# Kernel tuning notes

Measured on AMD Instinct MI355X. Metric: run time of the kernel, lower is better.

The kernel has to match this reference:

```python
import jax, jax.numpy as jnp
import numpy as np

NPG = 400          # nodes per graph (CC400 atlas ROIs)
B = 512            # graphs per batch
N = B * NPG        # total nodes
EPG = 6400         # edges per graph (avg degree 16)
E = B * EPG
F_IN = 200         # node feature dim
H = 64             # hidden_channels
C = 2              # num_classes


def _lin(k, fi, fo):
    return jax.random.normal(k, (fi, fo), jnp.float32) / np.sqrt(fi)


def setup_inputs() -> dict:
    key = jax.random.key(0)
    ks = jax.random.split(key, 16)
    # intra-graph edges: local src/dst in [0, NPG) plus per-graph offset
    g = jnp.repeat(jnp.arange(B, dtype=jnp.int32), EPG)
    src = jax.random.randint(ks[0], (E,), 0, NPG, dtype=jnp.int32) + g * NPG
    dst = jax.random.randint(ks[1], (E,), 0, NPG, dtype=jnp.int32) + g * NPG
    edge_index = jnp.stack([src, dst])  # [2, E]
    x = jax.random.normal(ks[2], (N, F_IN), jnp.float32)
    return dict(
        x=x, edge_index=edge_index, npg=NPG,
        # SAGEConv i: out = lin_l(mean_agg) + lin_r(x); lin_l carries the bias
        W1l=_lin(ks[3], F_IN, H), W1r=_lin(ks[4], F_IN, H), b1=jnp.zeros((H,), jnp.float32),
        W2l=_lin(ks[5], H, H), W2r=_lin(ks[6], H, H), b2=jnp.zeros((H,), jnp.float32),
        W3l=_lin(ks[7], H, H), W3r=_lin(ks[8], H, H), b3=jnp.zeros((H,), jnp.float32),
        # SAGPooling score GNN = GraphConv(H, 1): lin_rel(sum_agg) + lin_root(x)
        Wpr=_lin(ks[9], H, 1), bpr=jnp.zeros((1,), jnp.float32), Wpo=_lin(ks[10], H, 1),
        # final classifier
        Wlin=_lin(ks[11], H, C), blin=jnp.zeros((C,), jnp.float32),
    )


def reference(x, edge_index, npg, W1l, W1r, b1, W2l, W2r, b2, W3l, W3r, b3,
              Wpr, bpr, Wpo, Wlin, blin):
    n = x.shape[0]
    src, dst = edge_index[0], edge_index[1]

    deg = jax.ops.segment_sum(jnp.ones((src.shape[0],), x.dtype), dst, num_segments=n)
    inv_deg = 1.0 / jnp.maximum(deg, 1.0)  # [n]

    def sage(h, Wl, Wr, b):
        # mean aggregation over incoming edges, then lin_l(agg)+b + lin_r(h)
        agg = jax.ops.segment_sum(h[src], dst, num_segments=n) * inv_deg[:, None]
        return agg @ Wl + b + h @ Wr

    x1 = jax.nn.relu(sage(x, W1l, W1r, b1))
    x2 = jax.nn.relu(sage(x1, W2l, W2r, b2)) + x1
    x3 = jax.nn.relu(sage(x2, W3l, W3r, b3)) + x2

    # SAGPooling score via GraphConv (add aggregation)
    score = (jax.ops.segment_sum(x3[src], dst, num_segments=n) @ Wpr + bpr
             + x3 @ Wpo)[:, 0]  # [n]

    nb = n // npg            # number of graphs
    k = npg // 2             # ratio = 0.5, uniform graph sizes
    vals, idx = jax.lax.top_k(score.reshape(nb, npg), k)       # [nb, k]
    flat_idx = (jnp.arange(nb, dtype=idx.dtype)[:, None] * npg + idx).reshape(-1)
    xp = x3[flat_idx] * jnp.tanh(vals.reshape(-1))[:, None]    # [nb*k, H]

    pooled = xp.reshape(nb, k, -1).mean(axis=1)                # global_mean_pool
    logits = pooled @ Wlin + blin
    return jax.nn.log_softmax(logits, axis=1)
```

## Files before the change

### kernel.cpp

```cpp
#include <hip/hip_runtime.h>
#include <hip/hip_bf16.h>
#include <math.h>

#define F_IN 200
#define HDIM 64
#define NPG  400
#define EPG  6400
#define KSEL 200

typedef __attribute__((ext_vector_type(4))) float f32x4;
typedef __attribute__((ext_vector_type(8))) short s16x8;

__device__ __forceinline__ void gload_lds16(const void* g, void* l) {
    __builtin_amdgcn_global_load_lds(
        (const __attribute__((address_space(1))) void*)g,
        (__attribute__((address_space(3))) void*)l, 16, 0, 0);
}

__device__ __forceinline__ unsigned int bf16_rne(float x) {
    unsigned int b = __float_as_uint(x);
    return (b + 0x7FFFu + ((b >> 16) & 1u)) >> 16;
}

__device__ __forceinline__ void split8(f32x4 v0, f32x4 v1, s16x8& h, s16x8& l) {
    float x[8] = {v0.x, v0.y, v0.z, v0.w, v1.x, v1.y, v1.z, v1.w};
#pragma unroll
    for (int j = 0; j < 8; j++) {
        unsigned int hb = bf16_rne(x[j]);
        float hf = __uint_as_float(hb << 16);
        float r = x[j] - hf;
        unsigned int lb = bf16_rne(r);
        h[j] = (short)hb;
        l[j] = (short)lb;
    }
}

__global__ void pack_wf(const float* __restrict__ Wl, const float* __restrict__ Wr,
                        short* __restrict__ WF, int K, int KC) {
    int idx = blockIdx.x * blockDim.x + threadIdx.x;
    if (idx >= KC * 4096) return;
    int j    = idx & 7;
    int lane = (idx >> 3) & 63;
    int nf   = (idx >> 9) & 7;
    int kc   = idx >> 12;
    int k = kc * 32 + (lane >> 4) * 8 + j;
    int n = nf * 16 + (lane & 15);
    float v = 0.f;
    if (k < K) v = (n < 64) ? Wl[k * 64 + n] : Wr[k * 64 + (n - 64)];
    unsigned int hb = bf16_rne(v);
    float hf = __uint_as_float(hb << 16);
    unsigned int lb = bf16_rne(v - hf);
    WF[(size_t)((kc * 8 + nf) * 2 + 0) * 512 + lane * 8 + j] = (short)hb;
    WF[(size_t)((kc * 8 + nf) * 2 + 1) * 512 + lane * 8 + j] = (short)lb;
}

__global__ void pack_wf4(const float* __restrict__ Wl, const float* __restrict__ Wr,
                         short* __restrict__ WF) {
    int idx = blockIdx.x * blockDim.x + threadIdx.x;
    if (idx >= 4 * 2048) return;
    int j    = idx & 7;
    int lane = (idx >> 3) & 63;
    int nf   = (idx >> 9) & 3;
    int kc   = idx >> 11;
    int k = kc * 32 + (lane >> 4) * 8 + j;
    int n = nf * 16 + (lane & 15);
    float v = (k < 64) ? Wl[k * 64 + n] : Wr[(k - 64) * 64 + n];
    unsigned int hb = bf16_rne(v);
    float hf = __uint_as_float(hb << 16);
    unsigned int lb = bf16_rne(v - hf);
    WF[(size_t)((kc * 4 + nf) * 2 + 0) * 512 + lane * 8 + j] = (short)hb;
    WF[(size_t)((kc * 4 + nf) * 2 + 1) * 512 + lane * 8 + j] = (short)lb;
}

template <int K, int LDX, int KC, int TAIL>
__global__ __launch_bounds__(256) void gemm_lds(const float* __restrict__ X,
                                                const short* __restrict__ WF,
                                                float* __restrict__ O) {
    __shared__ float Xs[2][128 * 32];
    __shared__ short Ws[2][8 * 2 * 512];
    const int tid  = threadIdx.x;
    const int lane = tid & 63;
    const int wave = tid >> 6;
    const size_t rowbase = (size_t)blockIdx.x * 128;
    const f32x4 zero4 = (f32x4){0.f, 0.f, 0.f, 0.f};

    const int srow_off = wave * 32 + (lane >> 3);
    const int sbyte    = 16 * ((lane & 7) ^ (lane >> 3));

#define DMA_CHUNK(b, kc_) {                                                      \
    _Pragma("unroll")                                                            \
    for (int j = 0; j < 4; j++) {                                                \
        const char* xsrc = (const char*)X +                                      \
            (rowbase + srow_off + j * 8) * (size_t)(LDX * 4) + (kc_) * 128 + sbyte; \
        gload_lds16(xsrc, (char*)&Xs[b][0] + wave * 4096 + j * 1024);            \
        const short* wsrc = WF + (size_t)(kc_) * 8192 + wave * 2048 + j * 512 + lane * 8; \
        gload_lds16(wsrc, (char*)&Ws[b][0] + wave * 4096 + j * 1024);            \
    } }

    f32x4 acc[2][8];
#pragma unroll
    for (int m = 0; m < 2; m++)
#pragma unroll
        for (int nf = 0; nf < 8; nf++) acc[m][nf] = zero4;

    DMA_CHUNK(0, 0);
    __syncthreads();

    for (int kc = 0; kc < KC; kc++) {
        const int b = kc & 1;
        if (kc + 1 < KC) DMA_CHUNK(b ^ 1, kc + 1);

        s16x8 ah[2], al[2];
#pragma unroll
        for (int m = 0; m < 2; m++) {
            const int lr = wave * 32 + m * 16 + (lane & 15);
            const int g0 = (lane >> 4) * 2;
            f32x4 v0 = *(const f32x4*)&Xs[b][lr * 32 + 4 * (g0 ^ (lane & 7))];
            f32x4 v1 = *(const f32x4*)&Xs[b][lr * 32 + 4 * ((g0 + 1) ^ (lane & 7))];
            split8(v0, v1, ah[m], al[m]);
        }
#pragma unroll
        for (int nf = 0; nf < 8; nf++) {
            s16x8 wh = *(const s16x8*)&Ws[b][(nf * 2 + 0) * 512 + lane * 8];
            s16x8 wl = *(const s16x8*)&Ws[b][(nf * 2 + 1) * 512 + lane * 8];
#pragma unroll
            for (int m = 0; m < 2; m++) {
                acc[m][nf] = __builtin_amdgcn_mfma_f32_16x16x32_bf16(ah[m], wh, acc[m][nf], 0, 0, 0);
                acc[m][nf] = __builtin_amdgcn_mfma_f32_16x16x32_bf16(al[m], wh, acc[m][nf], 0, 0, 0);
                acc[m][nf] = __builtin_amdgcn_mfma_f32_16x16x32_bf16(ah[m], wl, acc[m][nf], 0, 0, 0);
            }
        }
        __syncthreads();
    }
#undef DMA_CHUNK

    if constexpr (TAIL > 0) {
        s16x8 ah[2], al[2];
#pragma unroll
        for (int m = 0; m < 2; m++) {
            const size_t row = rowbase + wave * 32 + m * 16 + (lane & 15);
            const int k0 = KC * 32 + (lane >> 4) * 8;
            f32x4 v0 = (k0 + 4 <= K) ? *(const f32x4*)&X[row * (size_t)LDX + k0] : zero4;
            f32x4 v1 = (k0 + 8 <= K) ? *(const f32x4*)&X[row * (size_t)LDX + k0 + 4] : zero4;
            split8(v0, v1, ah[m], al[m]);
        }
#pragma unroll
        for (int nf = 0; nf < 8; nf++) {
            s16x8 wh = *(const s16x8*)&WF[(size_t)((KC * 8 + nf) * 2 + 0) * 512 + lane * 8];
            s16x8 wl = *(const s16x8*)&WF[(size_t)((KC * 8 + nf) * 2 + 1) * 512 + lane * 8];
#pragma unroll
            for (int m = 0; m < 2; m++) {
                acc[m][nf] = __builtin_amdgcn_mfma_f32_16x16x32_bf16(ah[m], wh, acc[m][nf], 0, 0, 0);
                acc[m][nf] = __builtin_amdgcn_mfma_f32_16x16x32_bf16(al[m], wh, acc[m][nf], 0, 0, 0);
                acc[m][nf] = __builtin_amdgcn_mfma_f32_16x16x32_bf16(ah[m], wl, acc[m][nf], 0, 0, 0);
            }
        }
    }

    float* cs0 = &Xs[0][wave * 1024];
    float* cs1 = &Xs[1][wave * 1024];
#pragma unroll
    for (int m = 0; m < 2; m++) {
        const int scol = lane & 15;
        const int srow = (lane >> 4) * 4;
#pragma unroll
        for (int nf = 0; nf < 8; nf++)
#pragma unroll
            for (int r = 0; r < 4; r++) {
                int cr = srow + r;
                float* p = (cr < 8) ? cs0 + cr * 128 : cs1 + (cr - 8) * 128;
                p[nf * 16 + scol] = acc[m][nf][r];
            }
#pragma unroll
        for (int ps = 0; ps < 8; ps++) {
            int row = ps * 2 + (lane >> 5);
            const float* p = (row < 8) ? cs0 + row * 128 : cs1 + (row - 8) * 128;
            f32x4 v = *(const f32x4*)&p[(lane & 31) * 4];
            *(f32x4*)&O[(rowbase + wave * 32 + m * 16 + row) * 128 + (lane & 31) * 4] = v;
        }
    }
}

__global__ __launch_bounds__(1024) void combine_gemm(
    const float* __restrict__ M, const float* __restrict__ H,
    const short* __restrict__ WF, const float* __restrict__ bias,
    const float* __restrict__ resid, float* __restrict__ P)
{
    __shared__ float Xs[2][256 * 32];
    __shared__ short Ws[2][4 * 2 * 512];
    const int tid  = threadIdx.x;
    const int lane = tid & 63;
    const int wave = tid >> 6;
    const size_t rowbase = (size_t)blockIdx.x * 256;

#define DMA_C(b, c_) {                                                           \
    const float* srcbuf_ = ((c_) < 2) ? M : H;                                   \
    _Pragma("unroll")                                                            \
    for (int i = 0; i < 2; i++) {                                                \
        int rr = i * 8 + (lane >> 3);                                            \
        int jj = (lane & 7) ^ (rr & 7);                                          \
        const char* src = (const char*)(srcbuf_ + (rowbase + wave * 16 + rr) * 64) \
                          + ((c_) & 1) * 128 + jj * 16;                          \
        gload_lds16(src, (char*)&Xs[b][0] + wave * 2048 + i * 1024 + lane * 16); \
    }                                                                            \
    if (tid < 512) {                                                             \
        const short* wsrc = WF + (size_t)(c_) * 4096 + tid * 8;                  \
        gload_lds16(wsrc, (char*)&Ws[b][0] + tid * 16);                          \
    } }

    f32x4 acc[4];
#pragma unroll
    for (int nf = 0; nf < 4; nf++) acc[nf] = (f32x4){0.f, 0.f, 0.f, 0.f};

    DMA_C(0, 0);
    __syncthreads();

    for (int c = 0; c < 4; c++) {
        const int b = c & 1;
        if (c + 1 < 4) DMA_C(b ^ 1, c + 1);

        const int r = lane & 15;
        const int j0 = (lane >> 4) * 2;
        const float* abase = &Xs[b][wave * 512 + r * 32];
        f32x4 v0 = *(const f32x4*)&abase[((j0    ) ^ (r & 7)) * 4];
        f32x4 v1 = *(const f32x4*)&abase[((j0 + 1) ^ (r & 7)) * 4];
        s16x8 ah, al;
        split8(v0, v1, ah, al);
#pragma unroll
        for (int nf = 0; nf < 4; nf++) {
            s16x8 wh = *(const s16x8*)&Ws[b][(nf * 2 + 0) * 512 + lane * 8];
            s16x8 wl = *(const s16x8*)&Ws[b][(nf * 2 + 1) * 512 + lane * 8];
            acc[nf] = __builtin_amdgcn_mfma_f32_16x16x32_bf16(ah, wh, acc[nf], 0, 0, 0);
            acc[nf] = __builtin_amdgcn_mfma_f32_16x16x32_bf16(al, wh, acc[nf], 0, 0, 0);
            acc[nf] = __builtin_amdgcn_mfma_f32_16x16x32_bf16(ah, wl, acc[nf], 0, 0, 0);
        }
        __syncthreads();
    }
#undef DMA_C

    {
        const int scol = lane & 15;
        const int srow = (lane >> 4) * 4;
#pragma unroll
        for (int nf = 0; nf < 4; nf++)
#pragma unroll
            for (int ri = 0; ri < 4; ri++) {
                int cr = srow + ri;
                float* p = (cr < 8) ? &Xs[0][wave * 512 + cr * 64]
                                    : &Xs[1][wave * 512 + (cr - 8) * 64];
                p[nf * 16 + scol] = acc[nf][ri];
            }
#pragma unroll
        for (int i = 0; i < 4; i++) {
            int row = i * 4 + (lane >> 4);
            int col = (lane & 15) * 4;
            const float* p = (row < 8) ? &Xs[0][wave * 512 + row * 64]
                                       : &Xs[1][wave * 512 + (row - 8) * 64];
            f32x4 v = *(const f32x4*)&p[col];
            size_t grow = rowbase + wave * 16 + row;
            f32x4 bb = *(const f32x4*)&bias[col];
            f32x4 rr = *(const f32x4*)&resid[grow * 64 + col];
            f32x4 o;
#pragma unroll
            for (int q = 0; q < 4; q++) o[q] = fmaxf(v[q] + bb[q], 0.f) + rr[q];
            *(f32x4*)&P[grow * 64 + col] = o;
        }
    }
}

__global__ __launch_bounds__(256) void csr_build(
    const int* __restrict__ esrc, const int* __restrict__ edst,
    int* __restrict__ csr_src, int* __restrict__ rowptr,
    int* __restrict__ degs, float* __restrict__ invdeg)
{
    __shared__ int cnt[NPG];
    __shared__ int off[NPG];
    __shared__ int cur[NPG];
    const int g = blockIdx.x, tid = threadIdx.x;
    const int ebase = g * EPG, nodebase = g * NPG;
    for (int i = tid; i < NPG; i += 256) cnt[i] = 0;
    __syncthreads();
    for (int e = tid; e < EPG; e += 256)
        atomicAdd(&cnt[edst[ebase + e] - nodebase], 1);
    __syncthreads();
    if (tid == 0) {
        int run = 0;
        for (int i = 0; i < NPG; i++) { off[i] = run; run += cnt[i]; }
    }
    __syncthreads();
    for (int i = tid; i < NPG; i += 256) {
        cur[i] = off[i];
        rowptr[nodebase + i] = off[i];
        degs[nodebase + i] = cnt[i];
        invdeg[nodebase + i] = 1.f / fmaxf((float)cnt[i], 1.f);
    }
    __syncthreads();
    for (int e = tid; e < EPG; e += 256) {
        int ld = edst[ebase + e] - nodebase;
        int p = atomicAdd(&cur[ld], 1);
        csr_src[ebase + p] = esrc[ebase + e] - nodebase;
    }
}

__global__ __launch_bounds__(1024) void agg_lds(
    const float* __restrict__ A,
    const int* __restrict__ csr_src, const int* __restrict__ rowptr,
    const int* __restrict__ degs, const float* __restrict__ invdeg,
    const float* __restrict__ bias,
    float* __restrict__ Xout)
{
    __shared__ float y[NPG * 64];
    __shared__ int   csr_l[EPG];
    const int g = blockIdx.x, tid = threadIdx.x;
    const int ebase = g * EPG, nodebase = g * NPG;

    for (int idx = tid; idx < NPG * 16; idx += 1024) {
        int node = idx >> 4, c4 = (idx & 15) * 4;
        *(float4*)&y[node * 64 + c4] =
            *(const float4*)&A[(size_t)(nodebase + node) * 128 + c4];
    }
    for (int e = tid; e < EPG; e += 1024) csr_l[e] = csr_src[ebase + e];
    __syncthreads();

    const int wave = tid >> 6, lane = tid & 63;
    for (int node = wave; node < NPG; node += 16) {
        const int start = rowptr[nodebase + node];
        const int dg = degs[nodebase + node];
        float acc = 0.f;
        int j = 0;
        for (; j + 4 <= dg; j += 4) {
            int s0 = csr_l[start + j];
            int s1 = csr_l[start + j + 1];
            int s2 = csr_l[start + j + 2];
            int s3 = csr_l[start + j + 3];
            acc += y[s0 * 64 + lane] + y[s1 * 64 + lane]
                 + y[s2 * 64 + lane] + y[s3 * 64 + lane];
        }
        for (; j < dg; j++) acc += y[csr_l[start + j] * 64 + lane];

        float v = acc * invdeg[nodebase + node] + bias[lane]
                + A[(size_t)(nodebase + node) * 128 + 64 + lane];
        Xout[(size_t)(nodebase + node) * 64 + lane] = fmaxf(v, 0.f);
    }
}

__global__ __launch_bounds__(1024) void agg_in(
    const float* __restrict__ H,
    const int* __restrict__ csr_src, const int* __restrict__ rowptr,
    const int* __restrict__ degs, const float* __restrict__ invdeg,
    float* __restrict__ M)
{
    __shared__ float y[NPG * 64];
    __shared__ int   csr_l[EPG];
    const int g = blockIdx.x, tid = threadIdx.x;
    const int ebase = g * EPG, nodebase = g * NPG;

    for (int idx = tid; idx < NPG * 16; idx += 1024) {
        int node = idx >> 4, c4 = (idx & 15) * 4;
        *(float4*)&y[node * 64 + c4] =
            *(const float4*)&H[(size_t)(nodebase + node) * 64 + c4];
    }
    for (int e = tid; e < EPG; e += 1024) csr_l[e] = csr_src[ebase + e];
    __syncthreads();

    const int wave = tid >> 6, lane = tid & 63;
    for (int node = wave; node < NPG; node += 16) {
        const int start = rowptr[nodebase + node];
        const int dg = degs[nodebase + node];
        float acc = 0.f;
        int j = 0;
        for (; j + 4 <= dg; j += 4) {
            int s0 = csr_l[start + j];
            int s1 = csr_l[start + j + 1];
            int s2 = csr_l[start + j + 2];
            int s3 = csr_l[start + j + 3];
            acc += y[s0 * 64 + lane] + y[s1 * 64 + lane]
                 + y[s2 * 64 + lane] + y[s3 * 64 + lane];
        }
        for (; j < dg; j++) acc += y[csr_l[start + j] * 64 + lane];

        M[(size_t)(nodebase + node) * 64 + lane] = acc * invdeg[nodebase + node];
    }
}

__global__ __launch_bounds__(256) void score_pool(
    const float* __restrict__ X3,
    const int* __restrict__ esrc, const int* __restrict__ edst,
    const float* __restrict__ Wpr, const float* __restrict__ bpr,
    const float* __restrict__ Wpo,
    const float* __restrict__ Wlin, const float* __restrict__ blin,
    float* __restrict__ out)
{
    __shared__ float t0[NPG], s[NPG], w[NPG];
    __shared__ float wpr[64], wpo[64];
    __shared__ float pp[4 * 64];
    __shared__ float pooled[64];
    __shared__ float lg[2];
    const int g = blockIdx.x, tid = threadIdx.x;
    if (tid < 64) { wpr[tid] = Wpr[tid]; wpo[tid] = Wpo[tid]; }
    __syncthreads();

    const int nodebase = g * NPG;
    for (int i = tid; i < NPG; i += 256) {
        const float* xr = &X3[(size_t)(nodebase + i) * 64];
        float a0 = 0.f, a1 = 0.f;
        for (int d = 0; d < 64; d++) { float x = xr[d]; a0 += x * wpr[d]; a1 += x * wpo[d]; }
        t0[i] = a0;
        s[i] = bpr[0] + a1;
    }
    __syncthreads();
    const int ebase = g * EPG;
    for (int e = tid; e < EPG; e += 256) {
        int ls = esrc[ebase + e] - nodebase;
        int ld = edst[ebase + e] - nodebase;
        atomicAdd(&s[ld], t0[ls]);
    }
    __syncthreads();
    for (int i = tid; i < NPG; i += 256) {
        float si = s[i];
        int cnt = 0;
        for (int j = 0; j < NPG; j++) {
            float sj = s[j];
            cnt += (sj > si) || (sj == si && j < i);
        }
        w[i] = (cnt < KSEL) ? tanhf(si) * (1.f / KSEL) : 0.f;
    }
    __syncthreads();
    const int d = tid & 63, part = tid >> 6;
    float acc = 0.f;
    for (int i = part * 100; i < part * 100 + 100; i++)
        acc += w[i] * X3[(size_t)(nodebase + i) * 64 + d];
    pp[part * 64 + d] = acc;
    __syncthreads();
    if (tid < 64) pooled[tid] = pp[tid] + pp[64 + tid] + pp[128 + tid] + pp[192 + tid];
    __syncthreads();
    if (tid < 2) {
        float l = blin[tid];
        for (int dd = 0; dd < 64; dd++) l += pooled[dd] * Wlin[dd * 2 + tid];
        lg[tid] = l;
    }
    __syncthreads();
    if (tid < 2) {
        float m = fmaxf(lg[0], lg[1]);
        float lse = m + logf(expf(lg[0] - m) + expf(lg[1] - m));
        out[g * 2 + tid] = lg[tid] - lse;
    }
}

extern "C" void kernel_launch(void* const* d_in, const int* in_sizes, int n_in,
                              void* d_out, int out_size, void* d_ws, size_t ws_size,
                              hipStream_t stream) {
    const float* x    = (const float*)d_in[0];
    const int*   eidx = (const int*)d_in[1];
    const float* W1l  = (const float*)d_in[3];
    const float* W1r  = (const float*)d_in[4];
    const float* b1   = (const float*)d_in[5];
    const float* W2l  = (const float*)d_in[6];
    const float* W2r  = (const float*)d_in[7];
    const float* b2   = (const float*)d_in[8];
    const float* W3l  = (const float*)d_in[9];
    const float* W3r  = (const float*)d_in[10];
    const float* b3   = (const float*)d_in[11];
    const float* Wpr  = (const float*)d_in[12];
    const float* bpr  = (const float*)d_in[13];
    const float* Wpo  = (const float*)d_in[14];
    const float* Wlin = (const float*)d_in[15];
    const float* blin = (const float*)d_in[16];

    const int N = in_sizes[0] / F_IN;
    const int E = in_sizes[1] / 2;
    const int B = N / NPG;
    const int* esrc = eidx;
    const int* edst = eidx + E;

    float* ws = (float*)d_ws;
    float* A      = ws;
    float* P0     = A + (size_t)N * 128;
    float* P1     = P0 + (size_t)N * 64;
    float* Mb     = P1 + (size_t)N * 64;
    float* invdeg = Mb + (size_t)N * 64;
    short* WF1    = (short*)(invdeg + N);
    short* WFc2   = WF1 + 57344;
    short* WFc3   = WFc2 + 16384;
    int*   csr    = (int*)(WFc3 + 16384);
    int*   rowptr = csr + E;
    int*   degs   = rowptr + N;

    pack_wf<<<(7 * 4096 + 255) / 256, 256, 0, stream>>>(W1l, W1r, WF1, 200, 7);
    pack_wf4<<<(4 * 2048 + 255) / 256, 256, 0, stream>>>(W2l, W2r, WFc2);
    pack_wf4<<<(4 * 2048 + 255) / 256, 256, 0, stream>>>(W3l, W3r, WFc3);

    csr_build<<<B, 256, 0, stream>>>(esrc, edst, csr, rowptr, degs, invdeg);

    gemm_lds<200, 200, 6, 8><<<N / 128, 256, 0, stream>>>(x, WF1, A);
    agg_lds<<<B, 1024, 0, stream>>>(A, csr, rowptr, degs, invdeg, b1, P0);

    agg_in<<<B, 1024, 0, stream>>>(P0, csr, rowptr, degs, invdeg, Mb);
    combine_gemm<<<N / 256, 1024, 0, stream>>>(Mb, P0, WFc2, b2, P0, P1);

    agg_in<<<B, 1024, 0, stream>>>(P1, csr, rowptr, degs, invdeg, Mb);
    combine_gemm<<<N / 256, 1024, 0, stream>>>(Mb, P1, WFc3, b3, P1, P0);

    score_pool<<<B, 256, 0, stream>>>(P0, esrc, edst, Wpr, bpr, Wpo, Wlin, blin,
                                      (float*)d_out);
}
```

Before: 466.0 us.

## Rewrite score/pool kernel with wave-per-node reductions and CSR gather

The final scoring and pooling kernel now runs 1024 threads per graph. Each wave computes per-node dot products with coalesced row loads and shuffle reductions, where the old code had each thread loop serially over a 64-wide row. The edge scatter with shared-memory atomics is replaced by a CSR gather over a tile of source indices staged in LDS. The weighted pooling is also split across 16 waves. The intent is to remove strided per-thread row reads and atomic contention, at the cost of more LDS use and larger blocks.

```diff
diff --git a/kernel.cpp b/kernel.cpp
--- a/kernel.cpp
+++ b/kernel.cpp
@@ -383,67 +383,77 @@
     }
 }
 
-__global__ __launch_bounds__(256) void score_pool(
+__global__ __launch_bounds__(1024) void score_pool2(
     const float* __restrict__ X3,
-    const int* __restrict__ esrc, const int* __restrict__ edst,
+    const int* __restrict__ csr_src, const int* __restrict__ rowptr,
+    const int* __restrict__ degs,
     const float* __restrict__ Wpr, const float* __restrict__ bpr,
     const float* __restrict__ Wpo,
     const float* __restrict__ Wlin, const float* __restrict__ blin,
     float* __restrict__ out)
 {
-    __shared__ float t0[NPG], s[NPG], w[NPG];
-    __shared__ float wpr[64], wpo[64];
-    __shared__ float pp[4 * 64];
+    __shared__ int   csr_l[EPG];
+    __shared__ float t0s[NPG], ss[NPG], wsel[NPG];
+    __shared__ float pp[16 * 64];
     __shared__ float pooled[64];
-    __shared__ float lg[2];
+    __shared__ float lgs[2];
     const int g = blockIdx.x, tid = threadIdx.x;
-    if (tid < 64) { wpr[tid] = Wpr[tid]; wpo[tid] = Wpo[tid]; }
-    __syncthreads();
-
-    const int nodebase = g * NPG;
-    for (int i = tid; i < NPG; i += 256) {
-        const float* xr = &X3[(size_t)(nodebase + i) * 64];
-        float a0 = 0.f, a1 = 0.f;
-        for (int d = 0; d < 64; d++) { float x = xr[d]; a0 += x * wpr[d]; a1 += x * wpo[d]; }
-        t0[i] = a0;
-        s[i] = bpr[0] + a1;
-    }
-    __syncthreads();
-    const int ebase = g * EPG;
-    for (int e = tid; e < EPG; e += 256) {
-        int ls = esrc[ebase + e] - nodebase;
-        int ld = edst[ebase + e] - nodebase;
-        atomicAdd(&s[ld], t0[ls]);
-    }
-    __syncthreads();
-    for (int i = tid; i < NPG; i += 256) {
-        float si = s[i];
+    const int wave = tid >> 6, lane = tid & 63;
+    const int nodebase = g * NPG, ebase = g * EPG;
+
+    for (int e = tid; e < EPG; e += 1024) csr_l[e] = csr_src[ebase + e];
+
+    const float wpr = Wpr[lane], wpo = Wpo[lane];
+    for (int node = wave; node < NPG; node += 16) {
+        float v = X3[(size_t)(nodebase + node) * 64 + lane];
+        float a = v * wpr, b = v * wpo;
+#pragma unroll
+        for (int o = 32; o; o >>= 1) { a += __shfl_xor(a, o); b += __shfl_xor(b, o); }
+        if (lane == 0) { t0s[node] = a; ss[node] = bpr[0] + b; }
+    }
+    __syncthreads();
+    for (int node = wave; node < NPG; node += 16) {
+        const int start = rowptr[nodebase + node];
+        const int dg = degs[nodebase + node];
+        float a = 0.f;
+        for (int j = lane; j < dg; j += 64) a += t0s[csr_l[start + j]];
+#pragma unroll
+        for (int o = 32; o; o >>= 1) a += __shfl_xor(a, o);
+        if (lane == 0) ss[node] += a;
+    }
+    __syncthreads();
+    if (tid < NPG) {
+        float si = ss[tid];
         int cnt = 0;
         for (int j = 0; j < NPG; j++) {
-            float sj = s[j];
-            cnt += (sj > si) || (sj == si && j < i);
-        }
-        w[i] = (cnt < KSEL) ? tanhf(si) * (1.f / KSEL) : 0.f;
-    }
-    __syncthreads();
-    const int d = tid & 63, part = tid >> 6;
-    float acc = 0.f;
-    for (int i = part * 100; i < part * 100 + 100; i++)
-        acc += w[i] * X3[(size_t)(nodebase + i) * 64 + d];
-    pp[part * 64 + d] = acc;
-    __syncthreads();
-    if (tid < 64) pooled[tid] = pp[tid] + pp[64 + tid] + pp[128 + tid] + pp[192 + tid];
+            float sj = ss[j];
+            cnt += (sj > si) || (sj == si && j < tid);
+        }
+        wsel[tid] = (cnt < KSEL) ? tanhf(si) * (1.f / KSEL) : 0.f;
+    }
+    __syncthreads();
+    float a = 0.f;
+    for (int node = wave; node < NPG; node += 16)
+        a += wsel[node] * X3[(size_t)(nodebase + node) * 64 + lane];
+    pp[wave * 64 + lane] = a;
+    __syncthreads();
+    if (tid < 64) {
+        float s = 0.f;
+#pragma unroll
+        for (int i = 0; i < 16; i++) s += pp[i * 64 + tid];
+        pooled[tid] = s;
+    }
     __syncthreads();
     if (tid < 2) {
         float l = blin[tid];
-        for (int dd = 0; dd < 64; dd++) l += pooled[dd] * Wlin[dd * 2 + tid];
-        lg[tid] = l;
+        for (int d = 0; d < 64; d++) l += pooled[d] * Wlin[d * 2 + tid];
+        lgs[tid] = l;
     }
     __syncthreads();
     if (tid < 2) {
-        float m = fmaxf(lg[0], lg[1]);
-        float lse = m + logf(expf(lg[0] - m) + expf(lg[1] - m));
-        out[g * 2 + tid] = lg[tid] - lse;
+        float m = fmaxf(lgs[0], lgs[1]);
+        float lse = m + logf(expf(lgs[0] - m) + expf(lgs[1] - m));
+        out[g * 2 + tid] = lgs[tid] - lse;
     }
 }
 
@@ -501,6 +511,7 @@
     agg_in<<<B, 1024, 0, stream>>>(P1, csr, rowptr, degs, invdeg, Mb);
     combine_gemm<<<N / 256, 1024, 0, stream>>>(Mb, P1, WFc3, b3, P1, P0);
 
-    score_pool<<<B, 256, 0, stream>>>(P0, esrc, edst, Wpr, bpr, Wpo, Wlin, blin,
-                                      (float*)d_out);
-}
+    score_pool2<<<B, 1024, 0, stream>>>(P0, csr, rowptr, degs,
+                                        Wpr, bpr, Wpo, Wlin, blin,
+                                        (float*)d_out);
+}
```

Result: slower. 525.9 us (+12.9%).
